# Optimization experiments

Hardware: AMD Instinct MI355X
Metric: run time of the kernel (lower is better)

## Reference

```python
import math
import jax, jax.numpy as jnp
import numpy as np

B, S, D, H = 2, 4096, 1024, 16
HD = D // H            # 64 head dim
FFN = 4096             # encoder_ffn_dim = 4*d_model
WIN = 512              # attention_window
w = WIN // 2           # one-sided window = 256
NEG = -1e9


def setup_inputs() -> dict:
    key = jax.random.key(0)
    ks = jax.random.split(key, 16)
    p = lambda k, shape: (jax.random.normal(k, shape, jnp.float32) * 0.02)
    inp = {
        "hidden_states": jax.random.normal(ks[0], (B, S, D), jnp.float32),
        "attention_mask": jnp.zeros((B, S), jnp.float32),
        "layer_head_mask": jnp.ones((H,), jnp.float32),
        "is_index_masked": jnp.zeros((B, S), bool),
        "is_index_global_attn": jnp.zeros((B, S), bool),
        "is_global_attn": 0,
        "Wq": p(ks[1], (D, D)), "bq": jnp.zeros((D,), jnp.float32),
        "Wk": p(ks[2], (D, D)), "bk": jnp.zeros((D,), jnp.float32),
        "Wv": p(ks[3], (D, D)), "bv": jnp.zeros((D,), jnp.float32),
        "Wo": p(ks[4], (D, D)), "bo": jnp.zeros((D,), jnp.float32),
        "ln1_g": jnp.ones((D,), jnp.float32), "ln1_b": jnp.zeros((D,), jnp.float32),
        "W1": p(ks[5], (D, FFN)), "b1": jnp.zeros((FFN,), jnp.float32),
        "W2": p(ks[6], (FFN, D)), "b2": jnp.zeros((D,), jnp.float32),
        "ln2_g": jnp.ones((D,), jnp.float32), "ln2_b": jnp.zeros((D,), jnp.float32),
    }
    return inp


def _ln(x, g, b, eps=1e-5):
    m = x.mean(-1, keepdims=True)
    v = ((x - m) ** 2).mean(-1, keepdims=True)
    return (x - m) * jax.lax.rsqrt(v + eps) * g + b


def _blocks3(x, nb, pad_val=0.0):
    # x: [B, H, S, d] -> [B, H, nb, 3w, d]: key blocks b-1, b, b+1 per query block b
    xp = jnp.pad(x, ((0, 0), (0, 0), (w, w), (0, 0)), constant_values=pad_val)
    xb = xp.reshape(x.shape[0], x.shape[1], nb + 2, w, x.shape[-1])
    return jnp.concatenate([xb[:, :, i:i + nb] for i in range(3)], axis=3)


def _sliding_window_attn(q, k, v, key_mask_add, is_masked_q, head_mask):
    # q,k,v: [B, H, S, hd]; banded attention |i-j| <= w
    b, h, s, hd = q.shape
    nb = s // w
    qb = (q * (1.0 / math.sqrt(hd))).reshape(b, h, nb, w, hd)
    kb = _blocks3(k, nb)
    vb = _blocks3(v, nb)
    scores = jnp.einsum("bhnqd,bhnkd->bhnqk", qb, kb)  # [B,H,nb,w,3w]
    # additive key mask (padding keys get NEG)
    kmp = jnp.pad(key_mask_add, ((0, 0), (w, w)), constant_values=NEG)
    kmp = kmp.reshape(b, nb + 2, w)
    km = jnp.concatenate([kmp[:, i:i + nb] for i in range(3)], axis=2)  # [B,nb,3w]
    scores = scores + km[:, None, :, None, :]
    qi = jnp.arange(w)[:, None]
    ki = jnp.arange(3 * w)[None, :]
    band = jnp.abs(ki - w - qi) <= w  # [w, 3w]
    scores = jnp.where(band, scores, NEG)
    probs = jax.nn.softmax(scores, axis=-1)
    probs = probs * head_mask[None, :, None, None, None]
    probs = jnp.where(is_masked_q.reshape(b, 1, nb, w, 1), 0.0, probs)
    out = jnp.einsum("bhnqk,bhnkd->bhnqd", probs, vb)
    return out.reshape(b, h, s, hd)


def reference(hidden_states, attention_mask, layer_head_mask, is_index_masked,
              is_index_global_attn, is_global_attn,
              Wq, bq, Wk, bk, Wv, bv, Wo, bo, ln1_g, ln1_b,
              W1, b1, W2, b2, ln2_g, ln2_b):
    hs = hidden_states
    split = lambda x: (x).reshape(B, S, H, HD).transpose(0, 2, 1, 3)  # [B,H,S,hd]
    q = split(hs @ Wq + bq)
    k = split(hs @ Wk + bk)
    v = split(hs @ Wv + bv)
    attn = _sliding_window_attn(q, k, v, attention_mask, is_index_masked, layer_head_mask)
    attn = attn.transpose(0, 2, 1, 3).reshape(B, S, D)
    attn = attn @ Wo + bo  # self_attn output projection
    x = _ln(hs + attn, ln1_g, ln1_b)
    h = jax.nn.gelu(x @ W1 + b1, approximate=False)
    h = h @ W2 + b2
    x = _ln(x + h, ln2_g, ln2_b)
    return x
```

## Files before the change

kernel.cpp:

```cpp
#include <hip/hip_runtime.h>


typedef unsigned short ushort_t;
typedef unsigned char uchar_t;
typedef __attribute__((ext_vector_type(8))) short bf16x8;
typedef __attribute__((ext_vector_type(4))) float f32x4;

constexpr int CB  = 2;
constexpr int CS  = 4096;
constexpr int CD  = 1024;
constexpr int CH  = 16;
constexpr int CHD = 64;
constexpr int CF  = 4096;
constexpr int CM  = CB * CS;
constexpr float NEGV = -1e9f;

__device__ __forceinline__ ushort_t f2bf(float f) {
  unsigned u = __float_as_uint(f);
  unsigned r = u + 0x7FFFu + ((u >> 16) & 1u);
  return (ushort_t)(r >> 16);
}
__device__ __forceinline__ float gelu_exact(float x) {
  return 0.5f * x * (1.0f + erff(x * 0.70710678118654752f));
}

template <int NROWS>
__device__ __forceinline__ void stage_swz(const ushort_t* __restrict__ src, int stride,
                                          char* lds, int tid) {
  const int lane = tid & 63, w = tid >> 6;
#pragma unroll
  for (int it = 0; it < NROWS / 32; ++it) {
    const int o   = it * 4096 + w * 1024;
    const int eo  = o + lane * 16;
    const int row = eo >> 7;
    const int lslot = ((eo >> 4) & 7) ^ (row & 7);
    const ushort_t* g = src + (size_t)row * stride + lslot * 8;
    __builtin_amdgcn_global_load_lds((const __attribute__((address_space(1))) void*)g,
                                     (__attribute__((address_space(3))) void*)(lds + o),
                                     16, 0, 0);
  }
}

__device__ __forceinline__ bf16x8 ldsfrag(const char* lds, int row, int slot) {
  return *(const bf16x8*)(lds + row * 128 + (((slot ^ (row & 7)) << 4)));
}

__device__ __forceinline__ void mfma_mainloop(const ushort_t* __restrict__ A,
                                              const ushort_t* __restrict__ Bt,
                                              int K, int bm, int bn, int tid,
                                              char* As, char* Bs, f32x4 (&acc)[4][4]) {
  const int lane = tid & 63;
  const int wr = tid >> 7, wc = (tid >> 6) & 1;
  for (int k0 = 0; k0 < K; k0 += 64) {
    __syncthreads();
    stage_swz<128>(A + (size_t)bm * K + k0, K, As, tid);
    stage_swz<128>(Bt + (size_t)bn * K + k0, K, Bs, tid);
    __syncthreads();
#pragma unroll
    for (int kk = 0; kk < 2; ++kk) {
      bf16x8 af[4], bfr[4];
#pragma unroll
      for (int m = 0; m < 4; ++m)
        af[m] = ldsfrag(As, wr * 64 + m * 16 + (lane & 15), kk * 4 + (lane >> 4));
#pragma unroll
      for (int n = 0; n < 4; ++n)
        bfr[n] = ldsfrag(Bs, wc * 64 + n * 16 + (lane & 15), kk * 4 + (lane >> 4));
#pragma unroll
      for (int m = 0; m < 4; ++m)
#pragma unroll
        for (int n = 0; n < 4; ++n)
          acc[m][n] = __builtin_amdgcn_mfma_f32_16x16x32_bf16(af[m], bfr[n], acc[m][n], 0, 0, 0);
    }
  }
}

__global__ __launch_bounds__(256) void cast_bf16(const float* __restrict__ x,
                                                 ushort_t* __restrict__ y) {
  const size_t i = ((size_t)blockIdx.x * 256 + threadIdx.x) * 4;
  const float4 v = *(const float4*)(x + i);
  ushort4 o;
  o.x = f2bf(v.x); o.y = f2bf(v.y); o.z = f2bf(v.z); o.w = f2bf(v.w);
  *(ushort4*)(y + i) = o;
}

__global__ __launch_bounds__(256) void transpose_cast(const float* __restrict__ W,
                                                      ushort_t* __restrict__ Wt,
                                                      int K, int N) {
  __shared__ float t[64][65];
  const int k0 = blockIdx.x * 64, n0 = blockIdx.y * 64;
  const int ty = threadIdx.x >> 4, tx = threadIdx.x & 15;
#pragma unroll
  for (int rr = 0; rr < 4; ++rr) {
    const int r = rr * 16 + ty;
    const float4 v = *(const float4*)&W[(size_t)(k0 + r) * N + n0 + tx * 4];
    t[r][tx * 4 + 0] = v.x; t[r][tx * 4 + 1] = v.y;
    t[r][tx * 4 + 2] = v.z; t[r][tx * 4 + 3] = v.w;
  }
  __syncthreads();
#pragma unroll
  for (int rr = 0; rr < 4; ++rr) {
    const int rn = rr * 16 + ty;
    ushort4 o;
    o.x = f2bf(t[tx * 4 + 0][rn]); o.y = f2bf(t[tx * 4 + 1][rn]);
    o.z = f2bf(t[tx * 4 + 2][rn]); o.w = f2bf(t[tx * 4 + 3][rn]);
    *(ushort4*)&Wt[(size_t)(n0 + rn) * K + k0 + tx * 4] = o;
  }
}

__global__ __launch_bounds__(256) void gemm_qkv(
    const ushort_t* __restrict__ hsb,
    const ushort_t* __restrict__ WqT, const ushort_t* __restrict__ WkT,
    const ushort_t* __restrict__ WvT,
    const float* __restrict__ bq, const float* __restrict__ bk, const float* __restrict__ bv,
    ushort_t* __restrict__ q, ushort_t* __restrict__ k, ushort_t* __restrict__ vt) {
  __shared__ __align__(16) char As[16384];
  __shared__ __align__(16) char Bs[16384];
  const int tid = threadIdx.x, lane = tid & 63;
  const int wr = tid >> 7, wc = (tid >> 6) & 1;
  const int which = blockIdx.z;
  const ushort_t* Wt = (which == 0) ? WqT : (which == 1) ? WkT : WvT;
  const float* bia   = (which == 0) ? bq  : (which == 1) ? bk  : bv;
  const float mul    = (which == 0) ? 0.125f : 1.0f;
  const int bm = blockIdx.x * 128, bn = blockIdx.y * 128;

  f32x4 acc[4][4] = {};
  mfma_mainloop(hsb, Wt, CD, bm, bn, tid, As, Bs, acc);

#pragma unroll
  for (int m = 0; m < 4; ++m) {
#pragma unroll
    for (int n = 0; n < 4; ++n) {
      const int col = bn + wc * 64 + n * 16 + (lane & 15);
      const int h = col >> 6, hd = col & 63;
      const float bb = bia[col];
      const int r0 = bm + wr * 64 + m * 16 + ((lane >> 4) << 2);
      const int bidx = r0 >> 12;
      const int s0 = r0 & (CS - 1);
      if (which < 2) {
        ushort_t* dst = (which == 0 ? q : k);
#pragma unroll
        for (int i = 0; i < 4; ++i) {
          const float v = (acc[m][n][i] + bb) * mul;
          dst[((((size_t)bidx * CH + h) * CS) + s0 + i) * CHD + hd] = f2bf(v);
        }
      } else {
        ushort4 o;
        o.x = f2bf(acc[m][n][0] + bb); o.y = f2bf(acc[m][n][1] + bb);
        o.z = f2bf(acc[m][n][2] + bb); o.w = f2bf(acc[m][n][3] + bb);
        *(ushort4*)&vt[(((size_t)bidx * CH + h) * CHD + hd) * CS + s0] = o;
      }
    }
  }
}

template <int EPI>
__global__ __launch_bounds__(256) void gemm_epi(
    const ushort_t* __restrict__ A, const ushort_t* __restrict__ Bt,
    const float* __restrict__ bias, const float* __restrict__ res,
    float* __restrict__ outF, ushort_t* __restrict__ outB, int N, int K) {
  __shared__ __align__(16) char As[16384];
  __shared__ __align__(16) char Bs[16384];
  const int tid = threadIdx.x, lane = tid & 63;
  const int wr = tid >> 7, wc = (tid >> 6) & 1;
  const int bm = blockIdx.x * 128, bn = blockIdx.y * 128;

  f32x4 acc[4][4] = {};
  mfma_mainloop(A, Bt, K, bm, bn, tid, As, Bs, acc);

#pragma unroll
  for (int m = 0; m < 4; ++m) {
#pragma unroll
    for (int n = 0; n < 4; ++n) {
      const int col = bn + wc * 64 + n * 16 + (lane & 15);
      const float bb = bias[col];
      const int r0 = bm + wr * 64 + m * 16 + ((lane >> 4) << 2);
#pragma unroll
      for (int i = 0; i < 4; ++i) {
        float v = acc[m][n][i] + bb;
        if (EPI == 1) {
          v += res[(size_t)(r0 + i) * N + col];
          outF[(size_t)(r0 + i) * N + col] = v;
        } else {
          outB[(size_t)(r0 + i) * N + col] = f2bf(gelu_exact(v));
        }
      }
    }
  }
}

__global__ __launch_bounds__(256) void attn_mfma(
    const ushort_t* __restrict__ qg, const ushort_t* __restrict__ kg,
    const ushort_t* __restrict__ vtg,
    const float* __restrict__ amask, const uchar_t* __restrict__ qmask,
    const float* __restrict__ hmask, ushort_t* __restrict__ outb) {
  __shared__ __align__(16) char Qs[8192];
  __shared__ __align__(16) char Ks[8192];
  __shared__ __align__(16) char Vt[8192];
  __shared__ __align__(16) char Ps[8192];
  const int qt0 = blockIdx.x * 64, h = blockIdx.y, b = blockIdx.z;
  const int tid = threadIdx.x, lane = tid & 63, w = tid >> 6;
  const size_t bh = (size_t)b * CH + h;

  stage_swz<64>(qg + (bh * CS + qt0) * CHD, CHD, Qs, tid);

  f32x4 O[4] = {};
  float m_run[4], l_run[4];
#pragma unroll
  for (int i = 0; i < 4; ++i) { m_run[i] = -INFINITY; l_run[i] = 0.f; }

  for (int c = 0; c < 9; ++c) {
    const int k0 = qt0 - 256 + c * 64;
    if (k0 < 0 || k0 >= CS) continue;
    __syncthreads();
    stage_swz<64>(kg + (bh * CS + k0) * CHD, CHD, Ks, tid);
    stage_swz<64>(vtg + bh * CHD * CS + k0, CS, Vt, tid);
    __syncthreads();

    f32x4 s[4] = {};
#pragma unroll
    for (int kk = 0; kk < 2; ++kk) {
      const bf16x8 a = ldsfrag(Qs, w * 16 + (lane & 15), kk * 4 + (lane >> 4));
#pragma unroll
      for (int n = 0; n < 4; ++n) {
        const bf16x8 bb = ldsfrag(Ks, n * 16 + (lane & 15), kk * 4 + (lane >> 4));
        s[n] = __builtin_amdgcn_mfma_f32_16x16x32_bf16(a, bb, s[n], 0, 0, 0);
      }
    }

    float kmv[4]; int keyc[4];
#pragma unroll
    for (int n = 0; n < 4; ++n) {
      keyc[n] = k0 + n * 16 + (lane & 15);
      kmv[n] = amask[(size_t)b * CS + keyc[n]];
    }
    const int qrb = qt0 + w * 16 + ((lane >> 4) << 2);
#pragma unroll
    for (int i = 0; i < 4; ++i) {
      const int qi = qrb + i;
      float mx = -INFINITY;
#pragma unroll
      for (int n = 0; n < 4; ++n) {
        const int d = keyc[n] - qi;
        float x = (d <= 256 && d >= -256) ? (s[n][i] + kmv[n]) : NEGV;
        s[n][i] = x;
        mx = fmaxf(mx, x);
      }
      mx = fmaxf(mx, __shfl_xor(mx, 1));
      mx = fmaxf(mx, __shfl_xor(mx, 2));
      mx = fmaxf(mx, __shfl_xor(mx, 4));
      mx = fmaxf(mx, __shfl_xor(mx, 8));
      const float m_new = fmaxf(m_run[i], mx);
      const float scf = expf(m_run[i] - m_new);
      float rs = 0.f;
#pragma unroll
      for (int n = 0; n < 4; ++n) {
        const float p = expf(s[n][i] - m_new);
        s[n][i] = p;
        rs += p;
      }
      rs += __shfl_xor(rs, 1); rs += __shfl_xor(rs, 2);
      rs += __shfl_xor(rs, 4); rs += __shfl_xor(rs, 8);
      l_run[i] = l_run[i] * scf + rs;
      m_run[i] = m_new;
#pragma unroll
      for (int n = 0; n < 4; ++n) O[n][i] *= scf;
      const int prow = w * 16 + ((lane >> 4) << 2) + i;
#pragma unroll
      for (int n = 0; n < 4; ++n) {
        const int pcol = n * 16 + (lane & 15);
        const int byte = prow * 128 + ((((pcol >> 3) ^ (prow & 7)) << 4)) + ((pcol & 7) << 1);
        *(ushort_t*)(Ps + byte) = f2bf(s[n][i]);
      }
    }
    __syncthreads();

#pragma unroll
    for (int kk = 0; kk < 2; ++kk) {
      const bf16x8 pa = ldsfrag(Ps, w * 16 + (lane & 15), kk * 4 + (lane >> 4));
#pragma unroll
      for (int nd = 0; nd < 4; ++nd) {
        const bf16x8 vv = ldsfrag(Vt, nd * 16 + (lane & 15), kk * 4 + (lane >> 4));
        O[nd] = __builtin_amdgcn_mfma_f32_16x16x32_bf16(pa, vv, O[nd], 0, 0, 0);
      }
    }
  }

  const float hm = hmask[h];
#pragma unroll
  for (int i = 0; i < 4; ++i) {
    const int qi = qt0 + w * 16 + ((lane >> 4) << 2) + i;
    const bool qm = qmask[(size_t)b * CS + qi] != 0;
    const float scl = (qm ? 0.f : hm) / fmaxf(l_run[i], 1e-30f);
#pragma unroll
    for (int nd = 0; nd < 4; ++nd) {
      const int col = h * CHD + nd * 16 + (lane & 15);
      outb[((size_t)b * CS + qi) * CD + col] = f2bf(O[nd][i] * scl);
    }
  }
}

__global__ __launch_bounds__(256) void ln_f32(const float* __restrict__ X,
                                              const float* __restrict__ g,
                                              const float* __restrict__ bt,
                                              float* __restrict__ Y,
                                              ushort_t* __restrict__ Yb) {
  const int row = blockIdx.x;
  const int tid = threadIdx.x;
  const float4 xv = *(const float4*)(X + (size_t)row * CD + (tid << 2));
  float s  = xv.x + xv.y + xv.z + xv.w;
  float s2 = xv.x * xv.x + xv.y * xv.y + xv.z * xv.z + xv.w * xv.w;
#pragma unroll
  for (int off = 32; off; off >>= 1) {
    s  += __shfl_xor(s, off);
    s2 += __shfl_xor(s2, off);
  }
  __shared__ float red[8];
  const int wv = tid >> 6;
  if ((tid & 63) == 0) { red[wv] = s; red[wv + 4] = s2; }
  __syncthreads();
  s  = red[0] + red[1] + red[2] + red[3];
  s2 = red[4] + red[5] + red[6] + red[7];
  const float mean = s * (1.f / CD);
  const float var  = s2 * (1.f / CD) - mean * mean;
  const float r = rsqrtf(var + 1e-5f);
  const float4 gv = *(const float4*)(g + (tid << 2));
  const float4 bv = *(const float4*)(bt + (tid << 2));
  float4 o;
  o.x = (xv.x - mean) * r * gv.x + bv.x;
  o.y = (xv.y - mean) * r * gv.y + bv.y;
  o.z = (xv.z - mean) * r * gv.z + bv.z;
  o.w = (xv.w - mean) * r * gv.w + bv.w;
  *(float4*)(Y + (size_t)row * CD + (tid << 2)) = o;
  if (Yb) {
    ushort4 ob;
    ob.x = f2bf(o.x); ob.y = f2bf(o.y); ob.z = f2bf(o.z); ob.w = f2bf(o.w);
    *(ushort4*)(Yb + (size_t)row * CD + (tid << 2)) = ob;
  }
}

extern "C" void kernel_launch(void* const* d_in, const int* in_sizes, int n_in,
                              void* d_out, int out_size, void* d_ws, size_t ws_size,
                              hipStream_t stream) {
  const float* hs    = (const float*)d_in[0];
  const float* amask = (const float*)d_in[1];
  const float* hmask = (const float*)d_in[2];
  const uchar_t* qmask = (const uchar_t*)d_in[3];
  const float* Wq = (const float*)d_in[6];
  const float* bq = (const float*)d_in[7];
  const float* Wk = (const float*)d_in[8];
  const float* bk = (const float*)d_in[9];
  const float* Wv = (const float*)d_in[10];
  const float* bv = (const float*)d_in[11];
  const float* Wo = (const float*)d_in[12];
  const float* bo = (const float*)d_in[13];
  const float* ln1g = (const float*)d_in[14];
  const float* ln1b = (const float*)d_in[15];
  const float* W1 = (const float*)d_in[16];
  const float* b1 = (const float*)d_in[17];
  const float* W2 = (const float*)d_in[18];
  const float* b2 = (const float*)d_in[19];
  const float* ln2g = (const float*)d_in[20];
  const float* ln2b = (const float*)d_in[21];

  char* ws = (char*)d_ws;
  const size_t MB = 1024 * 1024;
  ushort_t* hsb  = (ushort_t*)(ws);
  ushort_t* WqT  = (ushort_t*)(ws + 16 * MB);
  ushort_t* WkT  = (ushort_t*)(ws + 18 * MB);
  ushort_t* WvT  = (ushort_t*)(ws + 20 * MB);
  ushort_t* WoT  = (ushort_t*)(ws + 22 * MB);
  ushort_t* W1T  = (ushort_t*)(ws + 24 * MB);
  ushort_t* W2T  = (ushort_t*)(ws + 32 * MB);
  ushort_t* qb   = (ushort_t*)(ws + 40 * MB);
  ushort_t* kb   = (ushort_t*)(ws + 56 * MB);
  ushort_t* vtb  = (ushort_t*)(ws + 72 * MB);
  ushort_t* attb = (ushort_t*)(ws + 88 * MB);
  float*    tmp  = (float*)(ws + 104 * MB);
  float*    x1   = (float*)(ws + 40 * MB);
  ushort_t* x1b  = (ushort_t*)(ws + 72 * MB);
  ushort_t* hb   = (ushort_t*)(ws + 136 * MB);
  float*    outf = (float*)d_out;

  cast_bf16<<<(CM * CD) / 1024, 256, 0, stream>>>(hs, hsb);
  transpose_cast<<<dim3(CD / 64, CD / 64), 256, 0, stream>>>(Wq, WqT, CD, CD);
  transpose_cast<<<dim3(CD / 64, CD / 64), 256, 0, stream>>>(Wk, WkT, CD, CD);
  transpose_cast<<<dim3(CD / 64, CD / 64), 256, 0, stream>>>(Wv, WvT, CD, CD);
  transpose_cast<<<dim3(CD / 64, CD / 64), 256, 0, stream>>>(Wo, WoT, CD, CD);
  transpose_cast<<<dim3(CD / 64, CF / 64), 256, 0, stream>>>(W1, W1T, CD, CF);
  transpose_cast<<<dim3(CF / 64, CD / 64), 256, 0, stream>>>(W2, W2T, CF, CD);

  gemm_qkv<<<dim3(CM / 128, CD / 128, 3), 256, 0, stream>>>(
      hsb, WqT, WkT, WvT, bq, bk, bv, qb, kb, vtb);

  attn_mfma<<<dim3(CS / 64, CH, CB), 256, 0, stream>>>(
      qb, kb, vtb, amask, qmask, hmask, attb);

  gemm_epi<1><<<dim3(CM / 128, CD / 128), 256, 0, stream>>>(
      attb, WoT, bo, hs, tmp, nullptr, CD, CD);

  ln_f32<<<CM, 256, 0, stream>>>(tmp, ln1g, ln1b, x1, x1b);

  gemm_epi<2><<<dim3(CM / 128, CF / 128), 256, 0, stream>>>(
      x1b, W1T, b1, nullptr, nullptr, hb, CF, CD);

  gemm_epi<1><<<dim3(CM / 128, CD / 128), 256, 0, stream>>>(
      hb, W2T, b2, x1, outf, nullptr, CD, CF);

  ln_f32<<<CM, 256, 0, stream>>>(outf, ln2g, ln2b, outf, nullptr);
}
```

Baseline: 552.4 us.

## Replace GEMMs with 8-wave, larger-tile, double-buffered pipelined MFMA mainloop

All four GEMMs (QKV, output projection, FFN1, FFN2) move from 128x128 tiles with 4 waves and a single-buffered LDS loop to 256x128 or 256x256 tiles with 8 waves. The new mainloop double-buffers LDS and splits each K step into phases, so async global-to-LDS loads for the next tiles are issued between MFMA batches and synchronised with fine-grained vmcnt waits and raw barriers. It also raises MFMA priority with s_setprio. The aim is to hide global load latency and raise reuse per block, at the cost of much more LDS and registers per block (launch bounds 512,1) and fewer blocks in flight.

```diff
diff --git a/kernel.cpp b/kernel.cpp
--- a/kernel.cpp
+++ b/kernel.cpp
@@ -22,6 +22,10 @@
 }
 __device__ __forceinline__ float gelu_exact(float x) {
   return 0.5f * x * (1.0f + erff(x * 0.70710678118654752f));
+}
+
+__device__ __forceinline__ bf16x8 ldsfrag(const char* lds, int row, int slot) {
+  return *(const bf16x8*)(lds + row * 128 + (((slot ^ (row & 7)) << 4)));
 }
 
 template <int NROWS>
@@ -41,35 +45,184 @@
   }
 }
 
-__device__ __forceinline__ bf16x8 ldsfrag(const char* lds, int row, int slot) {
-  return *(const bf16x8*)(lds + row * 128 + (((slot ^ (row & 7)) << 4)));
-}
-
-__device__ __forceinline__ void mfma_mainloop(const ushort_t* __restrict__ A,
-                                              const ushort_t* __restrict__ Bt,
-                                              int K, int bm, int bn, int tid,
-                                              char* As, char* Bs, f32x4 (&acc)[4][4]) {
-  const int lane = tid & 63;
-  const int wr = tid >> 7, wc = (tid >> 6) & 1;
-  for (int k0 = 0; k0 < K; k0 += 64) {
-    __syncthreads();
-    stage_swz<128>(A + (size_t)bm * K + k0, K, As, tid);
-    stage_swz<128>(Bt + (size_t)bn * K + k0, K, Bs, tid);
-    __syncthreads();
-#pragma unroll
-    for (int kk = 0; kk < 2; ++kk) {
-      bf16x8 af[4], bfr[4];
-#pragma unroll
-      for (int m = 0; m < 4; ++m)
-        af[m] = ldsfrag(As, wr * 64 + m * 16 + (lane & 15), kk * 4 + (lane >> 4));
-#pragma unroll
-      for (int n = 0; n < 4; ++n)
-        bfr[n] = ldsfrag(Bs, wc * 64 + n * 16 + (lane & 15), kk * 4 + (lane >> 4));
-#pragma unroll
-      for (int m = 0; m < 4; ++m)
-#pragma unroll
-        for (int n = 0; n < 4; ++n)
-          acc[m][n] = __builtin_amdgcn_mfma_f32_16x16x32_bf16(af[m], bfr[n], acc[m][n], 0, 0, 0);
+__device__ __forceinline__ void stageC(const ushort_t* __restrict__ gtile, int ldK,
+                                       char* ldsT, int chunk, int tid) {
+  const int eo   = chunk * 8192 + tid * 16;
+  const int row  = eo >> 7;
+  const int slot = ((eo >> 4) & 7) ^ (row & 7);
+  __builtin_amdgcn_global_load_lds(
+      (const __attribute__((address_space(1))) void*)(gtile + (size_t)row * ldK + slot * 8),
+      (__attribute__((address_space(3))) void*)(ldsT + eo), 16, 0, 0);
+}
+
+template <int MH, int NH, int NPH, int NF, int VM, typename F>
+__device__ __forceinline__ void phase8(const char* Ax, const char* Bx,
+                                       int wr, int wc, int rl, int kl,
+                                       f32x4 (&acc)[8][NF], F stage) {
+  bf16x8 af[4][2], bfr[NPH][2];
+#pragma unroll
+  for (int mf = 0; mf < 4; ++mf)
+#pragma unroll
+    for (int kk = 0; kk < 2; ++kk)
+      af[mf][kk] = ldsfrag(Ax, wr * 128 + (MH * 4 + mf) * 16 + rl, kk * 4 + kl);
+#pragma unroll
+  for (int nf = 0; nf < NPH; ++nf)
+#pragma unroll
+    for (int kk = 0; kk < 2; ++kk)
+      bfr[nf][kk] = ldsfrag(Bx, wc * (NF * 16) + (NH * NPH + nf) * 16 + rl, kk * 4 + kl);
+  stage();
+  __builtin_amdgcn_s_barrier();
+  asm volatile("s_waitcnt lgkmcnt(0)" ::: "memory");
+  __builtin_amdgcn_s_setprio(1);
+#pragma unroll
+  for (int mf = 0; mf < 4; ++mf)
+#pragma unroll
+    for (int nf = 0; nf < NPH; ++nf)
+#pragma unroll
+      for (int kk = 0; kk < 2; ++kk)
+        acc[MH * 4 + mf][NH * NPH + nf] = __builtin_amdgcn_mfma_f32_16x16x32_bf16(
+            af[mf][kk], bfr[nf][kk], acc[MH * 4 + mf][NH * NPH + nf], 0, 0, 0);
+  __builtin_amdgcn_s_setprio(0);
+  if constexpr (VM == 1) asm volatile("s_waitcnt vmcnt(2)" ::: "memory");
+  if constexpr (VM == 2) asm volatile("s_waitcnt vmcnt(0)" ::: "memory");
+  __builtin_amdgcn_s_barrier();
+}
+
+template <int BN>
+__device__ __forceinline__ void run_mainloop(const ushort_t* __restrict__ A,
+                                             const ushort_t* __restrict__ Bt,
+                                             int K, int bm, int bn, char* lds, int tid,
+                                             f32x4 (&acc)[8][BN / 64]) {
+  constexpr int NF = BN / 64;
+  char* Ab0 = lds;
+  char* Bb0 = lds + 32768;
+  char* Ab1 = lds + 32768 + BN * 128;
+  char* Bb1 = Ab1 + 32768;
+  const int lane = tid & 63, wid = tid >> 6;
+  const int wr = wid >> 2, wc = wid & 3, rl = lane & 15, kl = lane >> 4;
+  const ushort_t* Ao = A + (size_t)bm * K;
+  const ushort_t* Bo = Bt + (size_t)bn * K;
+  const int NT = K >> 6;
+#pragma unroll
+  for (int c = 0; c < 4; ++c) stageC(Ao, K, Ab0, c, tid);
+#pragma unroll
+  for (int c = 0; c < NF; ++c) stageC(Bo, K, Bb0, c, tid);
+  if (NT > 1) {
+    stageC(Ao + 64, K, Ab1, 0, tid);
+    stageC(Ao + 64, K, Ab1, 2, tid);
+    asm volatile("s_waitcnt vmcnt(2)" ::: "memory");
+  } else {
+    asm volatile("s_waitcnt vmcnt(0)" ::: "memory");
+  }
+  __builtin_amdgcn_s_barrier();
+
+  for (int m = 0; m < NT; ++m) {
+    const int p = m & 1;
+    char* Ax = p ? Ab1 : Ab0;  char* Bx = p ? Bb1 : Bb0;
+    char* Axn = p ? Ab0 : Ab1; char* Bxn = p ? Bb0 : Bb1;
+    const bool s1 = (m + 1 < NT), s2 = (m + 2 < NT);
+    const ushort_t* An1 = Ao + (m + 1) * 64;
+    const ushort_t* Bn1 = Bo + (m + 1) * 64;
+    const ushort_t* An2 = Ao + (m + 2) * 64;
+    if constexpr (NF == 4) {
+      phase8<0, 0, 2, 4, 0>(Ax, Bx, wr, wc, rl, kl, acc, [&] {
+        if (s1) { stageC(An1, K, Axn, 1, tid); stageC(An1, K, Axn, 3, tid); } });
+      phase8<0, 1, 2, 4, 0>(Ax, Bx, wr, wc, rl, kl, acc, [&] {
+        if (s1) { stageC(Bn1, K, Bxn, 0, tid); stageC(Bn1, K, Bxn, 1, tid); } });
+      phase8<1, 0, 2, 4, 0>(Ax, Bx, wr, wc, rl, kl, acc, [&] {
+        if (s1) { stageC(Bn1, K, Bxn, 2, tid); stageC(Bn1, K, Bxn, 3, tid); } });
+      if (s2)      phase8<1, 1, 2, 4, 1>(Ax, Bx, wr, wc, rl, kl, acc, [&] {
+        stageC(An2, K, Ax, 0, tid); stageC(An2, K, Ax, 2, tid); });
+      else if (s1) phase8<1, 1, 2, 4, 2>(Ax, Bx, wr, wc, rl, kl, acc, [&] {});
+      else         phase8<1, 1, 2, 4, 0>(Ax, Bx, wr, wc, rl, kl, acc, [&] {});
+    } else {
+      phase8<0, 0, 2, 2, 0>(Ax, Bx, wr, wc, rl, kl, acc, [&] {
+        if (s1) { stageC(An1, K, Axn, 1, tid); stageC(An1, K, Axn, 3, tid);
+                  stageC(Bn1, K, Bxn, 0, tid); } });
+      if (s2)      phase8<1, 0, 2, 2, 1>(Ax, Bx, wr, wc, rl, kl, acc, [&] {
+        stageC(Bn1, K, Bxn, 1, tid);
+        stageC(An2, K, Ax, 0, tid); stageC(An2, K, Ax, 2, tid); });
+      else if (s1) phase8<1, 0, 2, 2, 2>(Ax, Bx, wr, wc, rl, kl, acc, [&] {
+        stageC(Bn1, K, Bxn, 1, tid); });
+      else         phase8<1, 0, 2, 2, 0>(Ax, Bx, wr, wc, rl, kl, acc, [&] {});
+    }
+  }
+}
+
+template <int BN, int EPI>
+__global__ __launch_bounds__(512, 1) void gemm8(
+    const ushort_t* __restrict__ A, const ushort_t* __restrict__ Bt,
+    const float* __restrict__ bias, const float* __restrict__ res,
+    float* __restrict__ outF, ushort_t* __restrict__ outB, int N, int K) {
+  constexpr int NF = BN / 64;
+  __shared__ __align__(16) char lds[2 * (32768 + BN * 128)];
+  const int tid = threadIdx.x;
+  const int bm = blockIdx.x * 256, bn = blockIdx.y * BN;
+  f32x4 acc[8][NF] = {};
+  run_mainloop<BN>(A, Bt, K, bm, bn, lds, tid, acc);
+  const int lane = tid & 63, wid = tid >> 6;
+  const int wr = wid >> 2, wc = wid & 3, rl = lane & 15, kl = lane >> 4;
+#pragma unroll
+  for (int mf = 0; mf < 8; ++mf) {
+    const int r0 = bm + wr * 128 + mf * 16 + kl * 4;
+#pragma unroll
+    for (int nf = 0; nf < NF; ++nf) {
+      const int col = bn + wc * (NF * 16) + nf * 16 + rl;
+      const float bb = bias[col];
+#pragma unroll
+      for (int i = 0; i < 4; ++i) {
+        float v = acc[mf][nf][i] + bb;
+        if (EPI == 1) {
+          v += res[(size_t)(r0 + i) * N + col];
+          outF[(size_t)(r0 + i) * N + col] = v;
+        } else {
+          outB[(size_t)(r0 + i) * N + col] = f2bf(gelu_exact(v));
+        }
+      }
+    }
+  }
+}
+
+__global__ __launch_bounds__(512, 1) void qkv8(
+    const ushort_t* __restrict__ hsb,
+    const ushort_t* __restrict__ WqT, const ushort_t* __restrict__ WkT,
+    const ushort_t* __restrict__ WvT,
+    const float* __restrict__ bq, const float* __restrict__ bk, const float* __restrict__ bv,
+    ushort_t* __restrict__ q, ushort_t* __restrict__ k, ushort_t* __restrict__ vt) {
+  __shared__ __align__(16) char lds[2 * (32768 + 16384)];
+  const int tid = threadIdx.x;
+  const int which = blockIdx.z;
+  const ushort_t* Wt = (which == 0) ? WqT : (which == 1) ? WkT : WvT;
+  const float* bia   = (which == 0) ? bq  : (which == 1) ? bk  : bv;
+  const float mul    = (which == 0) ? 0.125f : 1.0f;
+  const int bm = blockIdx.x * 256, bn = blockIdx.y * 128;
+  f32x4 acc[8][2] = {};
+  run_mainloop<128>(hsb, Wt, CD, bm, bn, lds, tid, acc);
+  const int lane = tid & 63, wid = tid >> 6;
+  const int wr = wid >> 2, wc = wid & 3, rl = lane & 15, kl = lane >> 4;
+#pragma unroll
+  for (int mf = 0; mf < 8; ++mf) {
+    const int r0 = bm + wr * 128 + mf * 16 + kl * 4;
+    const int bidx = r0 >> 12;
+    const int s0 = r0 & (CS - 1);
+#pragma unroll
+    for (int nf = 0; nf < 2; ++nf) {
+      const int col = bn + wc * 32 + nf * 16 + rl;
+      const int h = col >> 6, hd = col & 63;
+      const float bb = bia[col];
+      if (which < 2) {
+        ushort_t* dst = (which == 0 ? q : k);
+#pragma unroll
+        for (int i = 0; i < 4; ++i) {
+          const float v = (acc[mf][nf][i] + bb) * mul;
+          dst[((((size_t)bidx * CH + h) * CS) + s0 + i) * CHD + hd] = f2bf(v);
+        }
+      } else {
+        ushort4 o;
+        o.x = f2bf(acc[mf][nf][0] + bb); o.y = f2bf(acc[mf][nf][1] + bb);
+        o.z = f2bf(acc[mf][nf][2] + bb); o.w = f2bf(acc[mf][nf][3] + bb);
+        *(ushort4*)&vt[(((size_t)bidx * CH + h) * CHD + hd) * CS + s0] = o;
+      }
     }
   }
 }
@@ -104,87 +257,6 @@
     o.x = f2bf(t[tx * 4 + 0][rn]); o.y = f2bf(t[tx * 4 + 1][rn]);
     o.z = f2bf(t[tx * 4 + 2][rn]); o.w = f2bf(t[tx * 4 + 3][rn]);
     *(ushort4*)&Wt[(size_t)(n0 + rn) * K + k0 + tx * 4] = o;
-  }
-}
-
-__global__ __launch_bounds__(256) void gemm_qkv(
-    const ushort_t* __restrict__ hsb,
-    const ushort_t* __restrict__ WqT, const ushort_t* __restrict__ WkT,
-    const ushort_t* __restrict__ WvT,
-    const float* __restrict__ bq, const float* __restrict__ bk, const float* __restrict__ bv,
-    ushort_t* __restrict__ q, ushort_t* __restrict__ k, ushort_t* __restrict__ vt) {
-  __shared__ __align__(16) char As[16384];
-  __shared__ __align__(16) char Bs[16384];
-  const int tid = threadIdx.x, lane = tid & 63;
-  const int wr = tid >> 7, wc = (tid >> 6) & 1;
-  const int which = blockIdx.z;
-  const ushort_t* Wt = (which == 0) ? WqT : (which == 1) ? WkT : WvT;
-  const float* bia   = (which == 0) ? bq  : (which == 1) ? bk  : bv;
-  const float mul    = (which == 0) ? 0.125f : 1.0f;
-  const int bm = blockIdx.x * 128, bn = blockIdx.y * 128;
-
-  f32x4 acc[4][4] = {};
-  mfma_mainloop(hsb, Wt, CD, bm, bn, tid, As, Bs, acc);
-
-#pragma unroll
-  for (int m = 0; m < 4; ++m) {
-#pragma unroll
-    for (int n = 0; n < 4; ++n) {
-      const int col = bn + wc * 64 + n * 16 + (lane & 15);
-      const int h = col >> 6, hd = col & 63;
-      const float bb = bia[col];
-      const int r0 = bm + wr * 64 + m * 16 + ((lane >> 4) << 2);
-      const int bidx = r0 >> 12;
-      const int s0 = r0 & (CS - 1);
-      if (which < 2) {
-        ushort_t* dst = (which == 0 ? q : k);
-#pragma unroll
-        for (int i = 0; i < 4; ++i) {
-          const float v = (acc[m][n][i] + bb) * mul;
-          dst[((((size_t)bidx * CH + h) * CS) + s0 + i) * CHD + hd] = f2bf(v);
-        }
-      } else {
-        ushort4 o;
-        o.x = f2bf(acc[m][n][0] + bb); o.y = f2bf(acc[m][n][1] + bb);
-        o.z = f2bf(acc[m][n][2] + bb); o.w = f2bf(acc[m][n][3] + bb);
-        *(ushort4*)&vt[(((size_t)bidx * CH + h) * CHD + hd) * CS + s0] = o;
-      }
-    }
-  }
-}
-
-template <int EPI>
-__global__ __launch_bounds__(256) void gemm_epi(
-    const ushort_t* __restrict__ A, const ushort_t* __restrict__ Bt,
-    const float* __restrict__ bias, const float* __restrict__ res,
-    float* __restrict__ outF, ushort_t* __restrict__ outB, int N, int K) {
-  __shared__ __align__(16) char As[16384];
-  __shared__ __align__(16) char Bs[16384];
-  const int tid = threadIdx.x, lane = tid & 63;
-  const int wr = tid >> 7, wc = (tid >> 6) & 1;
-  const int bm = blockIdx.x * 128, bn = blockIdx.y * 128;
-
-  f32x4 acc[4][4] = {};
-  mfma_mainloop(A, Bt, K, bm, bn, tid, As, Bs, acc);
-
-#pragma unroll
-  for (int m = 0; m < 4; ++m) {
-#pragma unroll
-    for (int n = 0; n < 4; ++n) {
-      const int col = bn + wc * 64 + n * 16 + (lane & 15);
-      const float bb = bias[col];
-      const int r0 = bm + wr * 64 + m * 16 + ((lane >> 4) << 2);
-#pragma unroll
-      for (int i = 0; i < 4; ++i) {
-        float v = acc[m][n][i] + bb;
-        if (EPI == 1) {
-          v += res[(size_t)(r0 + i) * N + col];
-          outF[(size_t)(r0 + i) * N + col] = v;
-        } else {
-          outB[(size_t)(r0 + i) * N + col] = f2bf(gelu_exact(v));
-        }
-      }
-    }
   }
 }
 
@@ -389,21 +461,21 @@
   transpose_cast<<<dim3(CD / 64, CF / 64), 256, 0, stream>>>(W1, W1T, CD, CF);
   transpose_cast<<<dim3(CF / 64, CD / 64), 256, 0, stream>>>(W2, W2T, CF, CD);
 
-  gemm_qkv<<<dim3(CM / 128, CD / 128, 3), 256, 0, stream>>>(
+  qkv8<<<dim3(CM / 256, CD / 128, 3), 512, 0, stream>>>(
       hsb, WqT, WkT, WvT, bq, bk, bv, qb, kb, vtb);
 
   attn_mfma<<<dim3(CS / 64, CH, CB), 256, 0, stream>>>(
       qb, kb, vtb, amask, qmask, hmask, attb);
 
-  gemm_epi<1><<<dim3(CM / 128, CD / 128), 256, 0, stream>>>(
+  gemm8<128, 1><<<dim3(CM / 256, CD / 128), 512, 0, stream>>>(
       attb, WoT, bo, hs, tmp, nullptr, CD, CD);
 
   ln_f32<<<CM, 256, 0, stream>>>(tmp, ln1g, ln1b, x1, x1b);
 
-  gemm_epi<2><<<dim3(CM / 128, CF / 128), 256, 0, stream>>>(
+  gemm8<256, 2><<<dim3(CM / 256, CF / 256), 512, 0, stream>>>(
       x1b, W1T, b1, nullptr, nullptr, hb, CF, CD);
 
-  gemm_epi<1><<<dim3(CM / 128, CD / 128), 256, 0, stream>>>(
+  gemm8<128, 1><<<dim3(CM / 256, CD / 128), 512, 0, stream>>>(
       hb, W2T, b2, x1, outf, nullptr, CD, CF);
 
   ln_f32<<<CM, 256, 0, stream>>>(outf, ln2g, ln2b, outf, nullptr);
```

After: 569.2 us. 1.03x slower.
